# Kernel optimization log

Hardware: AMD Instinct MI355X
Metric: run time of the kernel (lower is better)

## Reference

```python
import jax, jax.numpy as jnp
from jax import lax
import numpy as np

NC = 80      # classes
NM = 32      # mask coefficients
N = 8400     # anchors/boxes
H = 640; W = 640          # output canvas (img_shape)
MH = 160; MW = 160        # prototype mask resolution (img/4)
K = 100                   # max detections after NMS (fixed for jit)
CONF = 0.4
IOU_T = 0.7


def setup_inputs() -> dict:
    key = jax.random.key(0)
    k1, k2, k3, k4, k5, k6 = jax.random.split(key, 6)
    # well-formed boxes x1,y1,x2,y2 in pixel coords
    x1 = jax.random.uniform(k1, (1, 1, N), minval=0.0, maxval=float(W - 120))
    y1 = jax.random.uniform(k2, (1, 1, N), minval=0.0, maxval=float(H - 120))
    wh = jax.random.uniform(k3, (1, 2, N), minval=16.0, maxval=112.0)
    boxes = jnp.concatenate([x1, y1, x1 + wh[:, 0:1], y1 + wh[:, 1:2]], axis=1)
    cls = jax.random.uniform(k4, (1, NC, N), minval=0.0, maxval=0.6)  # some exceed CONF
    coeffs = jax.random.normal(k5, (1, NM, N)) * 0.5
    detect = jnp.concatenate([boxes, cls, coeffs], axis=1)   # [1, 4+NC+NM, N]
    segment = jax.random.normal(k6, (1, NM, MH, MW))
    return {"detect": detect, "segment": segment}


def _per_image(d, proto):
    mi = 4 + NC
    d = d.T                              # [N, 4+NC+NM]
    boxes = d[:, :4]                     # x1,y1,x2,y2
    cls = d[:, 4:mi]
    scores = jnp.max(cls, axis=1)
    cids = jnp.argmax(cls, axis=1)
    coeffs = d[:, mi:]                   # [N, NM]
    valid = scores >= CONF
    # sort by confidence descending (invalid last)
    order = jnp.argsort(jnp.where(valid, -scores, jnp.inf))
    b = boxes[order]; s = scores[order]; v = valid[order]
    c = cids[order]; co = coeffs[order]
    idx = jnp.arange(N)
    area = (b[:, 2] - b[:, 0]) * (b[:, 3] - b[:, 1])
    # greedy class-agnostic NMS (sequential over sorted boxes, vectorized inner)
    def nms_step(keep, i):
        bi = b[i]
        ix1 = jnp.maximum(bi[0], b[:, 0]); iy1 = jnp.maximum(bi[1], b[:, 1])
        ix2 = jnp.minimum(bi[2], b[:, 2]); iy2 = jnp.minimum(bi[3], b[:, 3])
        inter = jnp.maximum(ix2 - ix1, 0.0) * jnp.maximum(iy2 - iy1, 0.0)
        iou = inter / (area[i] + area - inter)
        sup = (iou >= IOU_T) & (idx > i) & keep[i]
        return keep & ~sup, None
    keep, _ = lax.scan(nms_step, v, idx)
    # mask-coefficient matmul for ALL boxes (as in source: masks @ segment_reshaped)
    mlog = co @ proto.reshape(NM, -1)    # [N, MH*MW]
    kept_scores = jnp.where(keep, s, -1.0)
    topv, topi = lax.top_k(kept_scores, K)   # first K survivors (already score-sorted)
    valid_k = topv >= CONF
    bk = b[topi]; ck = c[topi]
    prob = jax.nn.sigmoid(mlog[topi].reshape(K, MH, MW))
    hard = (prob > 0.5).astype(prob.dtype)               # binarize at mask res
    up = jax.image.resize(hard, (K, H, W), method="bilinear")  # upsample to canvas
    maskk = up > 0.0
    ysg = jnp.arange(H)[:, None]; xsg = jnp.arange(W)[None, :]
    onehot = jax.nn.one_hot(ck, NC, dtype=jnp.float32)   # [K, NC]
    bi = bk.astype(jnp.int32)
    # paint objects in descending-score order; each box region is overwritten
    def paint(canvas, inp):
        box, m, oh, vv = inp
        inbox = (xsg >= box[0]) & (xsg < box[2]) & (ysg >= box[1]) & (ysg < box[3]) & vv
        canvas = jnp.where(inbox[..., None],
                           jnp.where((m & inbox)[..., None], oh, 0.0),
                           canvas)
        return canvas, None
    canvas0 = jnp.zeros((H, W, NC), dtype=jnp.float32)
    canvas, _ = lax.scan(paint, canvas0, (bi, maskk, onehot, valid_k))
    return canvas


def reference(detect, segment):
    return jax.vmap(_per_image)(detect, segment)   # [B, H, W, NC]
```

## Files before the change

### kernel.cpp

```cpp
#include <hip/hip_runtime.h>

#define NCLS 80
#define NMK  32
#define NB   8400
#define MH_  160
#define MP   25600
#define IH   640
#define IW   640
#define KTOP 100
#define CONFT 0.4f
#define IOUT 0.7f
#define T_PRE 960
#define TW   (T_PRE/64)

__global__ __launch_bounds__(256) void k_prep(const float* __restrict__ det,
    float* __restrict__ key, int* __restrict__ cid, int* __restrict__ rank,
    int* __restrict__ nvalid)
{
  int n = blockIdx.x*256 + threadIdx.x;
  if (n >= NB) return;
  float best = det[4*NB + n];
  int bc = 0;
  #pragma unroll 8
  for (int c = 1; c < NCLS; ++c){
    float v = det[(4+c)*NB + n];
    if (v > best){ best = v; bc = c; }
  }
  cid[n] = bc;
  bool valid = best >= CONFT;
  key[n] = valid ? -best : __builtin_inff();
  rank[n] = 0;
  unsigned long long bal = __ballot(valid);
  if ((threadIdx.x & 63) == 0) atomicAdd(nvalid, (int)__popcll(bal));
}

__global__ __launch_bounds__(256) void k_rank(const float* __restrict__ key, int* __restrict__ rank)
{
  __shared__ float tk[256];
  int n = blockIdx.x*256 + threadIdx.x;
  float kn = (n < NB) ? key[n] : 0.f;
  int j0 = blockIdx.y * 1050;
  int j1 = j0 + 1050;
  int part = 0;
  for (int t0 = j0; t0 < j1; t0 += 256){
    int j = t0 + threadIdx.x;
    tk[threadIdx.x] = (j < NB) ? key[j] : 0.f;
    __syncthreads();
    int lim = min(256, j1 - t0);
    for (int jj = 0; jj < lim; ++jj){
      float kj = tk[jj];
      int jg = t0 + jj;
      part += ((kj < kn) || (kj == kn && jg < n)) ? 1 : 0;
    }
    __syncthreads();
  }
  if (n < NB && part) atomicAdd(&rank[n], part);
}

__global__ __launch_bounds__(256) void k_scatter(const float* __restrict__ det,
    const int* __restrict__ cid, const int* __restrict__ rank,
    int* __restrict__ perm, int* __restrict__ scid, float4* __restrict__ sbox)
{
  int n = blockIdx.x*256 + threadIdx.x;
  if (n >= NB) return;
  int r = rank[n];
  perm[r] = n;
  scid[r] = cid[n];
  float4 b;
  b.x = det[0*NB + n]; b.y = det[1*NB + n];
  b.z = det[2*NB + n]; b.w = det[3*NB + n];
  sbox[r] = b;
}

__global__ __launch_bounds__(64) void k_supmat(const float4* __restrict__ sbox,
    unsigned long long* __restrict__ supmat)
{
  const int lane = threadIdx.x;
  const int ti = blockIdx.x;
  const int tj = blockIdx.y;
  float4 bj = sbox[tj*64 + lane];
  float aj = (bj.z - bj.x) * (bj.w - bj.y);
  float4 bi_all = sbox[ti*64 + lane];
  float ai_all  = (bi_all.z - bi_all.x) * (bi_all.w - bi_all.y);
  const int jg = tj*64 + lane;
  unsigned long long myrow = 0ull;
  #pragma unroll 4
  for (int ii = 0; ii < 64; ++ii){
    float bix = __shfl(bi_all.x, ii, 64);
    float biy = __shfl(bi_all.y, ii, 64);
    float biz = __shfl(bi_all.z, ii, 64);
    float biw = __shfl(bi_all.w, ii, 64);
    float ai  = __shfl(ai_all,  ii, 64);
    float ix1 = fmaxf(bix, bj.x), iy1 = fmaxf(biy, bj.y);
    float ix2 = fminf(biz, bj.z), iy2 = fminf(biw, bj.w);
    float inter = fmaxf(ix2 - ix1, 0.f) * fmaxf(iy2 - iy1, 0.f);
    bool sup = (jg > ti*64 + ii) && (inter / (ai + aj - inter) >= IOUT);
    unsigned long long bal = __ballot(sup);
    if (lane == ii) myrow = bal;
  }
  supmat[(size_t)(ti*64 + lane)*TW + tj] = myrow;
}

__device__ __forceinline__ unsigned long long shfl64(unsigned long long v, int src){
  int lo = __shfl((int)(unsigned)(v & 0xffffffffull), src, 64);
  int hi = __shfl((int)(unsigned)(v >> 32), src, 64);
  return ((unsigned long long)(unsigned)hi << 32) | (unsigned)lo;
}

__global__ __launch_bounds__(1024) void k_greedy(const float4* __restrict__ sbox,
    const int* __restrict__ scid, const int* __restrict__ perm,
    const unsigned long long* __restrict__ supmat, const int* __restrict__ nvalid,
    int* __restrict__ selorig, int4* __restrict__ selbox, int* __restrict__ selcid,
    int* __restrict__ nsel)
{
  __shared__ __align__(16) unsigned long long lsup[T_PRE*TW];
  __shared__ int keptpos[KTOP];
  __shared__ int s_found;
  const int tid = threadIdx.x;
  {
    const float4* g4 = (const float4*)supmat;
    float4* l4 = (float4*)lsup;
    for (int idx = tid; idx < (T_PRE*TW)/2; idx += 1024) l4[idx] = g4[idx];
  }
  __syncthreads();

  if (tid < 64){
    const int lane = tid;
    const int nv = *nvalid;
    unsigned long long keepw = 0ull;
    if (lane < TW){
      int nbits = nv - lane*64;
      if (nbits >= 64) keepw = ~0ull;
      else if (nbits > 0) keepw = (1ull << nbits) - 1ull;
    }
    int found = 0;
    int cw = 0;
    for (;;){
      int pos = -1;
      for (;;){
        unsigned long long w = shfl64(keepw, cw);
        if (w){ pos = (cw << 6) + (int)__builtin_ctzll(w); break; }
        if (++cw == TW) break;
      }
      if (pos < 0) break;
      if (lane == 0) keptpos[found] = pos;
      found++;
      if (found >= KTOP) break;
      if (lane == cw) keepw &= ~(1ull << (pos & 63));
      if (lane < TW) keepw &= ~lsup[pos*TW + lane];
    }
    if (found < KTOP && nv > T_PRE){
      float4 kbA = make_float4(0.f,0.f,0.f,0.f);
      float4 kbB = make_float4(0.f,0.f,0.f,0.f);
      if (lane < found)      kbA = sbox[keptpos[lane]];
      if (lane + 64 < found) kbB = sbox[keptpos[lane + 64]];
      for (int j = T_PRE; j < nv && found < KTOP; ++j){
        float4 bj = sbox[j];
        float ajj = (bj.z - bj.x) * (bj.w - bj.y);
        bool s = false;
        if (lane < found){
          float ka = (kbA.z - kbA.x) * (kbA.w - kbA.y);
          float ix1 = fmaxf(kbA.x, bj.x), iy1 = fmaxf(kbA.y, bj.y);
          float ix2 = fminf(kbA.z, bj.z), iy2 = fminf(kbA.w, bj.w);
          float inter = fmaxf(ix2 - ix1, 0.f) * fmaxf(iy2 - iy1, 0.f);
          s = inter / (ka + ajj - inter) >= IOUT;
        }
        if (lane + 64 < found){
          float ka = (kbB.z - kbB.x) * (kbB.w - kbB.y);
          float ix1 = fmaxf(kbB.x, bj.x), iy1 = fmaxf(kbB.y, bj.y);
          float ix2 = fminf(kbB.z, bj.z), iy2 = fminf(kbB.w, bj.w);
          float inter = fmaxf(ix2 - ix1, 0.f) * fmaxf(iy2 - iy1, 0.f);
          s = s || (inter / (ka + ajj - inter) >= IOUT);
        }
        if (!__ballot(s)){
          if (lane == 0) keptpos[found] = j;
          if (found < 64){ if (lane == found) kbA = bj; }
          else           { if (lane == found - 64) kbB = bj; }
          found++;
        }
      }
    }
    if (lane == 0) s_found = found;
  }
  __syncthreads();
  const int ns = s_found;
  if (tid < ns){
    int si = keptpos[tid];
    float4 b = sbox[si];
    selorig[tid] = perm[si];
    selbox[tid]  = make_int4((int)b.x, (int)b.y, (int)b.z, (int)b.w);
    selcid[tid]  = scid[si];
  }
  if (tid == 0) *nsel = ns;
}

__global__ __launch_bounds__(256) void k_mask(const float* __restrict__ det, const float* __restrict__ proto,
    const int* __restrict__ selorig, const int* __restrict__ nsel, unsigned int* __restrict__ hb)
{
  const int p    = blockIdx.x*256 + threadIdx.x;
  const int lane = threadIdx.x & 63;
  const int wword = (blockIdx.x*256 + (threadIdx.x & ~63)) >> 5;
  float pr[NMK];
  #pragma unroll
  for (int m = 0; m < NMK; ++m) pr[m] = proto[m*MP + p];
  const int ns = *nsel;
  const int k0 = blockIdx.y * 10;
  for (int kk = 0; kk < 10; ++kk){
    int k = k0 + kk;
    if (k >= ns) break;
    int so = selorig[k];
    const float* cf = det + 84*NB + so;
    float acc = 0.f;
    #pragma unroll
    for (int m = 0; m < NMK; ++m) acc = fmaf(cf[(size_t)m*NB], pr[m], acc);
    unsigned long long bal = __ballot(acc > 0.f);
    if (lane == 0)  hb[k*800 + wword]     = (unsigned int)bal;
    if (lane == 32) hb[k*800 + wword + 1] = (unsigned int)(bal >> 32);
  }
}

__global__ __launch_bounds__(256) void k_paint(const int4* __restrict__ selbox, const int* __restrict__ selcid,
    const int* __restrict__ nsel, const unsigned int* __restrict__ hb, float* __restrict__ out)
{
  __shared__ int4  sbx[KTOP];
  __shared__ int   scd[KTOP];
  __shared__ short wcls[IW];
  __shared__ short clist[KTOP];
  __shared__ int   ccount;
  const int y = blockIdx.x;
  const int tid = threadIdx.x;
  const int ns = *nsel;
  if (tid < ns){ sbx[tid] = selbox[tid]; scd[tid] = selcid[tid]; }
  if (tid == 0) ccount = 0;
  __syncthreads();
  if (tid == 0){
    int m = 0;
    for (int k = 0; k < ns; ++k)
      if (y >= sbx[k].y && y < sbx[k].w) clist[m++] = (short)k;
    ccount = m;
  }
  __syncthreads();
  const int m = ccount;
  const int fyi = (y - 2) >> 2;
  const int ylo = max(fyi, 0), yhi = min(fyi + 1, MH_ - 1);
  for (int x = tid; x < IW; x += 256){
    int cls = -1;
    for (int ci = m - 1; ci >= 0; --ci){
      int k = clist[ci];
      int4 b = sbx[k];
      if (x >= b.x && x < b.z){
        int fx = (x - 2) >> 2;
        int xlo = max(fx, 0), xhi = min(fx + 1, MH_ - 1);
        bool on = false;
        for (int ry = ylo; ry <= yhi; ++ry)
          for (int rx = xlo; rx <= xhi; ++rx){
            int pp = ry*MH_ + rx;
            on = on || ((hb[k*800 + (pp >> 5)] >> (pp & 31)) & 1u);
          }
        cls = on ? scd[k] : -1;
        break;
      }
    }
    wcls[x] = (short)cls;
  }
  __syncthreads();
  float4* o4 = (float4*)(out + (size_t)y * (IW*NCLS));
  for (int it = 0; it < 50; ++it){
    int f4 = it*256 + tid;
    int x  = f4 / 20;
    int c  = (f4 % 20) * 4;
    int wc = wcls[x];
    float4 v;
    v.x = (wc == c    ) ? 1.f : 0.f;
    v.y = (wc == c + 1) ? 1.f : 0.f;
    v.z = (wc == c + 2) ? 1.f : 0.f;
    v.w = (wc == c + 3) ? 1.f : 0.f;
    o4[f4] = v;
  }
}

extern "C" void kernel_launch(void* const* d_in, const int* in_sizes, int n_in,
                              void* d_out, int out_size, void* d_ws, size_t ws_size,
                              hipStream_t stream)
{
  const float* det   = (const float*)d_in[0];
  const float* proto = (const float*)d_in[1];
  float* out = (float*)d_out;
  char* w = (char*)d_ws;
  float*  key     = (float*)(w + 0);
  int*    cid     = (int*)  (w + 33600);
  int*    rank    = (int*)  (w + 67200);
  int*    perm    = (int*)  (w + 100800);
  int*    scid    = (int*)  (w + 134400);
  float4* sbox    = (float4*)(w + 168000);
  int*    selorig = (int*)  (w + 302400);
  int4*   selbox  = (int4*) (w + 302800);
  int*    selcid  = (int*)  (w + 304400);
  int*    nsel    = (int*)  (w + 304800);
  int*    nvalid  = (int*)  (w + 304804);
  unsigned int* hb = (unsigned int*)(w + 304816);
  unsigned long long* supmat = (unsigned long long*)(w + 304816);

  hipMemsetAsync(nvalid, 0, 4, stream);
  hipLaunchKernelGGL(k_prep,    dim3(33),      dim3(256),  0, stream, det, key, cid, rank, nvalid);
  hipLaunchKernelGGL(k_rank,    dim3(33, 8),   dim3(256),  0, stream, key, rank);
  hipLaunchKernelGGL(k_scatter, dim3(33),      dim3(256),  0, stream, det, cid, rank, perm, scid, sbox);
  hipLaunchKernelGGL(k_supmat,  dim3(15, 15),  dim3(64),   0, stream, sbox, supmat);
  hipLaunchKernelGGL(k_greedy,  dim3(1),       dim3(1024), 0, stream, sbox, scid, perm, supmat, nvalid,
                     selorig, selbox, selcid, nsel);
  hipLaunchKernelGGL(k_mask,    dim3(100, 10), dim3(256),  0, stream, det, proto, selorig, nsel, hb);
  hipLaunchKernelGGL(k_paint,   dim3(640),     dim3(256),  0, stream, selbox, selcid, nsel, hb, out);
}
```

Measured before the change: 250.6 us.

## Fuse suppression-matrix build and valid count into single-block greedy NMS kernel

Removes the separate k_supmat kernel and the nvalid memset/atomic: the single 1024-thread NMS block now counts valid boxes itself and builds the IoU suppression matrix straight into shared memory, with a smaller precomputed window (384 instead of 960). The greedy scan becomes a linear walk over candidates with prefetched suppression rows instead of a search for the next set bit. k_rank is split into 32 chunks instead of 8 for more parallelism, and k_mask handles 25 detections per block instead of 10. The aim is fewer launches and less global traffic. The risk is that a window this small sends more cases to the slow serial fallback loop, and the single block has to do all the matrix work.

```diff
diff --git a/kernel.cpp b/kernel.cpp
--- a/kernel.cpp
+++ b/kernel.cpp
@@ -10,12 +10,11 @@
 #define KTOP 100
 #define CONFT 0.4f
 #define IOUT 0.7f
-#define T_PRE 960
+#define T_PRE 384
 #define TW   (T_PRE/64)
 
 __global__ __launch_bounds__(256) void k_prep(const float* __restrict__ det,
-    float* __restrict__ key, int* __restrict__ cid, int* __restrict__ rank,
-    int* __restrict__ nvalid)
+    float* __restrict__ key, int* __restrict__ cid, int* __restrict__ rank)
 {
   int n = blockIdx.x*256 + threadIdx.x;
   if (n >= NB) return;
@@ -27,11 +26,8 @@
     if (v > best){ best = v; bc = c; }
   }
   cid[n] = bc;
-  bool valid = best >= CONFT;
-  key[n] = valid ? -best : __builtin_inff();
+  key[n] = (best >= CONFT) ? -best : __builtin_inff();
   rank[n] = 0;
-  unsigned long long bal = __ballot(valid);
-  if ((threadIdx.x & 63) == 0) atomicAdd(nvalid, (int)__popcll(bal));
 }
 
 __global__ __launch_bounds__(256) void k_rank(const float* __restrict__ key, int* __restrict__ rank)
@@ -39,8 +35,8 @@
   __shared__ float tk[256];
   int n = blockIdx.x*256 + threadIdx.x;
   float kn = (n < NB) ? key[n] : 0.f;
-  int j0 = blockIdx.y * 1050;
-  int j1 = j0 + 1050;
+  int j0 = blockIdx.y * 263;
+  int j1 = min(j0 + 263, NB);
   int part = 0;
   for (int t0 = j0; t0 < j1; t0 += 256){
     int j = t0 + threadIdx.x;
@@ -72,61 +68,56 @@
   sbox[r] = b;
 }
 
-__global__ __launch_bounds__(64) void k_supmat(const float4* __restrict__ sbox,
-    unsigned long long* __restrict__ supmat)
-{
-  const int lane = threadIdx.x;
-  const int ti = blockIdx.x;
-  const int tj = blockIdx.y;
-  float4 bj = sbox[tj*64 + lane];
-  float aj = (bj.z - bj.x) * (bj.w - bj.y);
-  float4 bi_all = sbox[ti*64 + lane];
-  float ai_all  = (bi_all.z - bi_all.x) * (bi_all.w - bi_all.y);
-  const int jg = tj*64 + lane;
-  unsigned long long myrow = 0ull;
-  #pragma unroll 4
-  for (int ii = 0; ii < 64; ++ii){
-    float bix = __shfl(bi_all.x, ii, 64);
-    float biy = __shfl(bi_all.y, ii, 64);
-    float biz = __shfl(bi_all.z, ii, 64);
-    float biw = __shfl(bi_all.w, ii, 64);
-    float ai  = __shfl(ai_all,  ii, 64);
-    float ix1 = fmaxf(bix, bj.x), iy1 = fmaxf(biy, bj.y);
-    float ix2 = fminf(biz, bj.z), iy2 = fminf(biw, bj.w);
-    float inter = fmaxf(ix2 - ix1, 0.f) * fmaxf(iy2 - iy1, 0.f);
-    bool sup = (jg > ti*64 + ii) && (inter / (ai + aj - inter) >= IOUT);
-    unsigned long long bal = __ballot(sup);
-    if (lane == ii) myrow = bal;
-  }
-  supmat[(size_t)(ti*64 + lane)*TW + tj] = myrow;
-}
-
-__device__ __forceinline__ unsigned long long shfl64(unsigned long long v, int src){
-  int lo = __shfl((int)(unsigned)(v & 0xffffffffull), src, 64);
-  int hi = __shfl((int)(unsigned)(v >> 32), src, 64);
-  return ((unsigned long long)(unsigned)hi << 32) | (unsigned)lo;
-}
-
-__global__ __launch_bounds__(1024) void k_greedy(const float4* __restrict__ sbox,
-    const int* __restrict__ scid, const int* __restrict__ perm,
-    const unsigned long long* __restrict__ supmat, const int* __restrict__ nvalid,
+__global__ __launch_bounds__(1024) void k_nms2(const float* __restrict__ key,
+    const float4* __restrict__ sbox, const int* __restrict__ scid, const int* __restrict__ perm,
     int* __restrict__ selorig, int4* __restrict__ selbox, int* __restrict__ selcid,
     int* __restrict__ nsel)
 {
   __shared__ __align__(16) unsigned long long lsup[T_PRE*TW];
   __shared__ int keptpos[KTOP];
+  __shared__ int s_nv;
   __shared__ int s_found;
-  const int tid = threadIdx.x;
+  const int tid  = threadIdx.x;
+  const int lane = tid & 63;
+  const int wv   = tid >> 6;
+  if (tid == 0) s_nv = 0;
+  __syncthreads();
   {
-    const float4* g4 = (const float4*)supmat;
-    float4* l4 = (float4*)lsup;
-    for (int idx = tid; idx < (T_PRE*TW)/2; idx += 1024) l4[idx] = g4[idx];
-  }
-  __syncthreads();
-
-  if (tid < 64){
-    const int lane = tid;
-    const int nv = *nvalid;
+    int cnt = 0;
+    for (int n = tid; n < NB; n += 1024){
+      unsigned long long bal = __ballot(key[n] < 1e38f);
+      if (lane == 0) cnt += (int)__popcll(bal);
+    }
+    if (lane == 0 && cnt) atomicAdd(&s_nv, cnt);
+  }
+  for (int t = wv; t < TW*TW; t += 16){
+    const int ti = t / TW, tj = t % TW;
+    float4 bj = sbox[tj*64 + lane];
+    float aj = (bj.z - bj.x) * (bj.w - bj.y);
+    float4 bi_all = sbox[ti*64 + lane];
+    float ai_all  = (bi_all.z - bi_all.x) * (bi_all.w - bi_all.y);
+    const int jg = tj*64 + lane;
+    unsigned long long myrow = 0ull;
+    #pragma unroll 4
+    for (int ii = 0; ii < 64; ++ii){
+      float bix = __shfl(bi_all.x, ii, 64);
+      float biy = __shfl(bi_all.y, ii, 64);
+      float biz = __shfl(bi_all.z, ii, 64);
+      float biw = __shfl(bi_all.w, ii, 64);
+      float ai  = __shfl(ai_all,  ii, 64);
+      float ix1 = fmaxf(bix, bj.x), iy1 = fmaxf(biy, bj.y);
+      float ix2 = fminf(biz, bj.z), iy2 = fminf(biw, bj.w);
+      float inter = fmaxf(ix2 - ix1, 0.f) * fmaxf(iy2 - iy1, 0.f);
+      bool sup = (jg > ti*64 + ii) && (inter / (ai + aj - inter) >= IOUT);
+      unsigned long long bal = __ballot(sup);
+      if (lane == ii) myrow = bal;
+    }
+    lsup[(ti*64 + lane)*TW + tj] = myrow;
+  }
+  __syncthreads();
+
+  if (wv == 0){
+    const int nv = s_nv;
     unsigned long long keepw = 0ull;
     if (lane < TW){
       int nbits = nv - lane*64;
@@ -134,20 +125,19 @@
       else if (nbits > 0) keepw = (1ull << nbits) - 1ull;
     }
     int found = 0;
-    int cw = 0;
-    for (;;){
-      int pos = -1;
-      for (;;){
-        unsigned long long w = shfl64(keepw, cw);
-        if (w){ pos = (cw << 6) + (int)__builtin_ctzll(w); break; }
-        if (++cw == TW) break;
+    const int lim = min(nv, T_PRE);
+    unsigned long long r0 = (lane < TW) ? lsup[0*TW + lane] : 0ull;
+    unsigned long long r1 = (lane < TW) ? lsup[1*TW + lane] : 0ull;
+    for (int cand = 0; cand < lim; ++cand){
+      unsigned long long r2 = (lane < TW && cand + 2 < T_PRE) ? lsup[(cand+2)*TW + lane] : 0ull;
+      bool mine = (lane == (cand >> 6)) && ((keepw >> (cand & 63)) & 1ull);
+      if (__ballot(mine)){
+        if (lane == 0) keptpos[found] = cand;
+        found++;
+        if (found >= KTOP) break;
+        keepw &= ~r0;
       }
-      if (pos < 0) break;
-      if (lane == 0) keptpos[found] = pos;
-      found++;
-      if (found >= KTOP) break;
-      if (lane == cw) keepw &= ~(1ull << (pos & 63));
-      if (lane < TW) keepw &= ~lsup[pos*TW + lane];
+      r0 = r1; r1 = r2;
     }
     if (found < KTOP && nv > T_PRE){
       float4 kbA = make_float4(0.f,0.f,0.f,0.f);
@@ -204,8 +194,8 @@
   #pragma unroll
   for (int m = 0; m < NMK; ++m) pr[m] = proto[m*MP + p];
   const int ns = *nsel;
-  const int k0 = blockIdx.y * 10;
-  for (int kk = 0; kk < 10; ++kk){
+  const int k0 = blockIdx.y * 25;
+  for (int kk = 0; kk < 25; ++kk){
     int k = k0 + kk;
     if (k >= ns) break;
     int so = selorig[k];
@@ -297,17 +287,13 @@
   int4*   selbox  = (int4*) (w + 302800);
   int*    selcid  = (int*)  (w + 304400);
   int*    nsel    = (int*)  (w + 304800);
-  int*    nvalid  = (int*)  (w + 304804);
   unsigned int* hb = (unsigned int*)(w + 304816);
-  unsigned long long* supmat = (unsigned long long*)(w + 304816);
-
-  hipMemsetAsync(nvalid, 0, 4, stream);
-  hipLaunchKernelGGL(k_prep,    dim3(33),      dim3(256),  0, stream, det, key, cid, rank, nvalid);
-  hipLaunchKernelGGL(k_rank,    dim3(33, 8),   dim3(256),  0, stream, key, rank);
+
+  hipLaunchKernelGGL(k_prep,    dim3(33),      dim3(256),  0, stream, det, key, cid, rank);
+  hipLaunchKernelGGL(k_rank,    dim3(33, 32),  dim3(256),  0, stream, key, rank);
   hipLaunchKernelGGL(k_scatter, dim3(33),      dim3(256),  0, stream, det, cid, rank, perm, scid, sbox);
-  hipLaunchKernelGGL(k_supmat,  dim3(15, 15),  dim3(64),   0, stream, sbox, supmat);
-  hipLaunchKernelGGL(k_greedy,  dim3(1),       dim3(1024), 0, stream, sbox, scid, perm, supmat, nvalid,
+  hipLaunchKernelGGL(k_nms2,    dim3(1),       dim3(1024), 0, stream, key, sbox, scid, perm,
                      selorig, selbox, selcid, nsel);
-  hipLaunchKernelGGL(k_mask,    dim3(100, 10), dim3(256),  0, stream, det, proto, selorig, nsel, hb);
+  hipLaunchKernelGGL(k_mask,    dim3(100, 4),  dim3(256),  0, stream, det, proto, selorig, nsel, hb);
   hipLaunchKernelGGL(k_paint,   dim3(640),     dim3(256),  0, stream, selbox, selcid, nsel, hb, out);
 }
```

After: 262.5 us. 1.05x slower.
